# Kernel tuning notes

Hardware: AMD Instinct MI355X
Metric: run time of the kernel (lower is better)

The kernel has to match this reference:

```python
import jax, jax.numpy as jnp
import numpy as np

N, F, H, OUT, DDIM, E = 200000, 64, 256, 16, 768, 3200000


def setup_inputs() -> dict:
    key = jax.random.key(0)
    ks = jax.random.split(key, 20)
    s = lambda i, shp, sc=0.05: (jax.random.normal(ks[i], shp, jnp.float32) * sc)
    return dict(
        x=jax.random.normal(ks[0], (N, F), jnp.float32),
        edge_index=jax.random.randint(ks[1], (2, E), 0, N, dtype=jnp.int32),
        doc_feature=jax.random.normal(ks[2], (DDIM,), jnp.float32),
        pool_w=s(3, (F,)),
        init_weight=s(4, (F, F)),
        gru_w_ih=s(5, (3 * F, F)), gru_w_hh=s(6, (3 * F, F)),
        gru_b_ih=s(7, (3 * F,)), gru_b_hh=s(8, (3 * F,)),
        gnn_fc_w=s(9, (H, F)), gnn_fc_b=s(10, (H,)),
        doc_fc_w=s(11, (H, DDIM)), doc_fc_b=s(12, (H,)),
        ln_g=jnp.ones((2 * H,), jnp.float32), ln_b=jnp.zeros((2 * H,), jnp.float32),
        fusion_w=s(13, (H, 2 * H)), fusion_b=s(14, (H,)),
        task_w=s(15, (OUT, H)), task_b=s(16, (OUT,)),
        time_w=s(17, (1, H)), time_b=s(18, (1,)),
    )


def _forward(x, doc_feature, pool_w, init_weight, gru_w_ih, gru_w_hh, gru_b_ih,
             gru_b_hh, gnn_fc_w, gnn_fc_b, doc_fc_w, doc_fc_b, ln_g, ln_b,
             fusion_w, fusion_b, task_w, task_b, time_w, time_b, edge_index):
    n, f = x.shape
    # --- EvolveGCNH: TopK pooling, k = f since ratio = in_channels/num_nodes ---
    score = x @ pool_w / jnp.linalg.norm(pool_w)             # [n]
    top_s, perm = jax.lax.top_k(score, f)
    x_tilde = x[perm] * jnp.tanh(top_s)[:, None]             # [f, f]
    # --- single-step GRU; hidden state = previous GCN weight (detached) ---
    h0 = jax.lax.stop_gradient(init_weight)                  # [f, f]
    gx = x_tilde @ gru_w_ih.T + gru_b_ih                     # [f, 3f]
    gh = h0 @ gru_w_hh.T + gru_b_hh
    xr, xz, xn = jnp.split(gx, 3, axis=1)
    hr, hz, hn = jnp.split(gh, 3, axis=1)
    r = jax.nn.sigmoid(xr + hr)
    z = jax.nn.sigmoid(xz + hz)
    nc = jnp.tanh(xn + r * hn)
    W = (1.0 - z) * nc + z * h0                              # evolved weight [f, f]
    # --- GCNConv with fixed W: sym-norm adjacency with self loops ---
    xw = x @ W                                               # [n, f]
    loop = jnp.arange(n, dtype=edge_index.dtype)
    row = jnp.concatenate([edge_index[0], loop])
    col = jnp.concatenate([edge_index[1], loop])
    deg = jax.ops.segment_sum(jnp.ones_like(col, dtype=x.dtype), col, num_segments=n)
    dis = jnp.where(deg > 0, jax.lax.rsqrt(jnp.maximum(deg, 1e-12)), 0.0)
    norm = dis[row] * dis[col]                               # [E+n]
    x_gnn = jax.ops.segment_sum(xw[row] * norm[:, None], col, num_segments=n)  # [n, f]
    # --- global mean pool (batch is all zeros -> single graph) ---
    pooled = jnp.mean(x_gnn, axis=0, keepdims=True)          # [1, f]
    g = pooled @ gnn_fc_w.T + gnn_fc_b                        # [1, H]
    d = jax.nn.relu(doc_feature @ doc_fc_w.T + doc_fc_b)[None, :]  # [1, H]
    fused = jnp.concatenate([g, d], axis=1)                   # [1, 2H]
    mu = jnp.mean(fused, axis=-1, keepdims=True)
    var = jnp.var(fused, axis=-1, keepdims=True)
    ln = (fused - mu) * jax.lax.rsqrt(var + 1e-5) * ln_g + ln_b
    h1 = jax.nn.relu(ln @ fusion_w.T + fusion_b)              # dropout = identity (eval)
    return (h1 @ task_w.T + task_b, h1 @ time_w.T + time_b)


def reference(x, edge_index, doc_feature, pool_w, init_weight, gru_w_ih, gru_w_hh,
              gru_b_ih, gru_b_hh, gnn_fc_w, gnn_fc_b, doc_fc_w, doc_fc_b, ln_g,
              ln_b, fusion_w, fusion_b, task_w, task_b, time_w, time_b):
    return _forward(x, doc_feature, pool_w, init_weight, gru_w_ih, gru_w_hh,
                    gru_b_ih, gru_b_hh, gnn_fc_w, gnn_fc_b, doc_fc_w, doc_fc_b,
                    ln_g, ln_b, fusion_w, fusion_b, task_w, task_b, time_w,
                    time_b, edge_index)
```

## Files before the change

kernel.cpp:

```cpp
#include <hip/hip_runtime.h>
#include <hip/hip_bf16.h>

#define NN    200000
#define EE    3200000
#define DDIMC 768

#define NI4   800000
#define HTH   1024
#define PARTW (25 * 12 * 8192)

#define BSZC  32768
#define BSHC  15
#define NBC   7
#define CCC   72
#define BSZR  16384
#define BSHR  14
#define NBR   13
#define CCR   40

#define NDBLK 782
#define XBLOCKS 1024
#define CAPL  4096

#define HB    64
#define HW    32768

#define P_PART  0
#define P_DEGM  P_PART
#define P_PARTM (P_DEGM + 114688)
#define PZERO_LEN 327680
#define P_HIST  PARTW
#define P_CANDN (P_HIST + 65536)
#define P_S8    (P_CANDN + 8)
#define ZERO_LEN (8 + 512)
#define P_FLAG  (P_S8 + 512)
#define P_THR   (P_FLAG + 8)
#define P_SV    (P_THR + 8)
#define P_D     (P_SV + 64)
#define P_DIS   (P_D + 256)
#define P_C     (P_DIS + NN)
#define P_SCORE (P_C + NN)
#define P_CKEY  (P_SCORE + NN)
#define P_CIDX  (P_CKEY + 4096)
#define P_XT    (P_CIDX + 4096)
#define P_WW    (P_XT + 4096)
#define P_G     (P_WW + 4096)
#define P_LNV   (P_G + 256)
#define P_H1    (P_LNV + 512)

__device__ __forceinline__ float ldf(const void* p, int i, int bf) {
  if (bf) return __bfloat162float(((const __hip_bfloat16*)p)[i]);
  return ((const float*)p)[i];
}
__device__ __forceinline__ void stf(void* p, int i, float v, int bf) {
  if (bf) ((__hip_bfloat16*)p)[i] = __float2bfloat16(v);
  else ((float*)p)[i] = v;
}
__device__ __forceinline__ float bfu(unsigned u) {
  return __uint_as_float(u << 16);
}
__device__ __forceinline__ float wsum(float v) {
#pragma unroll
  for (int m = 32; m >= 1; m >>= 1) v += __shfl_xor(v, m, 64);
  return v;
}
__device__ __forceinline__ int wsumi(int v) {
#pragma unroll
  for (int m = 32; m >= 1; m >>= 1) v += __shfl_xor(v, m, 64);
  return v;
}
__device__ __forceinline__ unsigned sortkey(float f) {
  unsigned u = __float_as_uint(f);
  return (u & 0x80000000u) ? ~u : (u | 0x80000000u);
}

__global__ void k_detect(const unsigned short* x16, int* flag) {
  __shared__ int cnt;
  if (threadIdx.x == 0) cnt = 0;
  __syncthreads();
  int ok = 0;
  for (int k = threadIdx.x; k < 512; k += 256) {
    unsigned short u = x16[2 * k];
    int e = (u >> 7) & 0xFF;
    if (u == 0 || (e >= 100 && e <= 150)) ok++;
  }
  atomicAdd(&cnt, ok);
  __syncthreads();
  if (threadIdx.x == 0) flag[0] = (cnt >= 400) ? 1 : 0;
}

__global__ void __launch_bounds__(HTH) k_hcol(const int* __restrict__ col,
                                              unsigned* __restrict__ degm) {
  __shared__ unsigned lh[BSZC / 2];
  int t = threadIdx.x;
  int b = blockIdx.x / CCC, j = blockIdx.x % CCC;
  for (int k = t; k < BSZC / 2; k += HTH) lh[k] = 0u;
  __syncthreads();
  int base = b << BSHC;
  const int4* c4 = (const int4*)col;
  const int stride = CCC * HTH;
  for (int i = j * HTH + t; i < NI4; i += 2 * stride) {
    int4 v0 = c4[i];
    int i2 = i + stride;
    int4 v1; v1.x = v1.y = v1.z = v1.w = -1;
    if (i2 < NI4) v1 = c4[i2];
    {
      int a0 = v0.x - base, a1 = v0.y - base, a2 = v0.z - base, a3 = v0.w - base;
      if ((unsigned)a0 < (unsigned)BSZC) atomicAdd(&lh[a0 >> 1], 1u << ((a0 & 1) * 16));
      if ((unsigned)a1 < (unsigned)BSZC) atomicAdd(&lh[a1 >> 1], 1u << ((a1 & 1) * 16));
      if ((unsigned)a2 < (unsigned)BSZC) atomicAdd(&lh[a2 >> 1], 1u << ((a2 & 1) * 16));
      if ((unsigned)a3 < (unsigned)BSZC) atomicAdd(&lh[a3 >> 1], 1u << ((a3 & 1) * 16));
    }
    {
      int a0 = v1.x - base, a1 = v1.y - base, a2 = v1.z - base, a3 = v1.w - base;
      if ((unsigned)a0 < (unsigned)BSZC) atomicAdd(&lh[a0 >> 1], 1u << ((a0 & 1) * 16));
      if ((unsigned)a1 < (unsigned)BSZC) atomicAdd(&lh[a1 >> 1], 1u << ((a1 & 1) * 16));
      if ((unsigned)a2 < (unsigned)BSZC) atomicAdd(&lh[a2 >> 1], 1u << ((a2 & 1) * 16));
      if ((unsigned)a3 < (unsigned)BSZC) atomicAdd(&lh[a3 >> 1], 1u << ((a3 & 1) * 16));
    }
  }
  __syncthreads();
  unsigned* dst = degm + (size_t)b * (BSZC / 2);
  for (int k = t; k < BSZC / 2; k += HTH) {
    unsigned v = lh[k];
    if (v) atomicAdd(&dst[k], v);
  }
}

__global__ void k_redA(const unsigned* __restrict__ degm, float* __restrict__ dis,
                       const void* docf, const void* dw, const void* db,
                       float* __restrict__ d, const int* flagp) {
  if (blockIdx.x < NDBLK) {
    int i = blockIdx.x * 256 + threadIdx.x;
    if (i < NN) {
      unsigned w_ = degm[i >> 1];
      int deg = 1 + (int)((w_ >> ((i & 1) * 16)) & 0xffffu);
      dis[i] = rsqrtf((float)deg);
    }
  } else {
    int flag = flagp[0];
    int o = (blockIdx.x - NDBLK) * 4 + (threadIdx.x >> 6);
    int lane = threadIdx.x & 63;
    float acc = 0.f;
    for (int k = lane; k < DDIMC; k += 64) acc += ldf(docf, k, flag) * ldf(dw, o * DDIMC + k, flag);
    acc = wsum(acc);
    if (lane == 0) d[o] = fmaxf(acc + ldf(db, o, flag), 0.0f);
  }
}

__global__ void __launch_bounds__(HTH) k_hrow(const int* __restrict__ row, const int* __restrict__ col,
                                              const float* __restrict__ dis,
                                              float* __restrict__ partm) {
  __shared__ float lh[BSZR];
  int t = threadIdx.x;
  int b = blockIdx.x / CCR, j = blockIdx.x % CCR;
  for (int k = t; k < BSZR; k += HTH) lh[k] = 0.f;
  __syncthreads();
  int base = b << BSHR;
  const int4* r4 = (const int4*)row;
  const int4* c4 = (const int4*)col;
  const int stride = CCR * HTH;
  for (int i = j * HTH + t; i < NI4; i += 2 * stride) {
    int4 r0 = r4[i];
    int4 c0 = c4[i];
    int i2 = i + stride;
    int4 r1; r1.x = r1.y = r1.z = r1.w = -1;
    int4 c1; c1.x = c1.y = c1.z = c1.w = 0;
    if (i2 < NI4) { r1 = r4[i2]; c1 = c4[i2]; }
    {
      int a0 = r0.x - base, a1 = r0.y - base, a2 = r0.z - base, a3 = r0.w - base;
      if ((unsigned)a0 < (unsigned)BSZR) atomicAdd(&lh[a0], dis[c0.x]);
      if ((unsigned)a1 < (unsigned)BSZR) atomicAdd(&lh[a1], dis[c0.y]);
      if ((unsigned)a2 < (unsigned)BSZR) atomicAdd(&lh[a2], dis[c0.z]);
      if ((unsigned)a3 < (unsigned)BSZR) atomicAdd(&lh[a3], dis[c0.w]);
    }
    {
      int a0 = r1.x - base, a1 = r1.y - base, a2 = r1.z - base, a3 = r1.w - base;
      if ((unsigned)a0 < (unsigned)BSZR) atomicAdd(&lh[a0], dis[c1.x]);
      if ((unsigned)a1 < (unsigned)BSZR) atomicAdd(&lh[a1], dis[c1.y]);
      if ((unsigned)a2 < (unsigned)BSZR) atomicAdd(&lh[a2], dis[c1.z]);
      if ((unsigned)a3 < (unsigned)BSZR) atomicAdd(&lh[a3], dis[c1.w]);
    }
  }
  __syncthreads();
  float* dst = partm + (size_t)b * BSZR;
  for (int k = t; k < BSZR; k += HTH) {
    float v = lh[k];
    if (v != 0.f) atomicAdd(&dst[k], v);
  }
}

__global__ void k_redB(const float* __restrict__ partm, const float* __restrict__ dis,
                       float* __restrict__ c) {
  int i = blockIdx.x * 256 + threadIdx.x;
  if (i < NN) {
    float dv = dis[i];
    c[i] = dv * partm[i] + dv * dv;
  }
}

__global__ void k_x(const void* x, const void* pw, const float* __restrict__ c,
                    float* __restrict__ score,
                    float* __restrict__ s8, const int* flagp) {
  __shared__ float sred[4][64];
  int flag = flagp[0];
  int t = threadIdx.x;
  int lane = t & 63;
  int w = t >> 6;
  int wid = (blockIdx.x * 256 + t) >> 6;
  int nw = (gridDim.x * 256) >> 6;

  if (flag) {
    int g  = lane >> 3;
    int c0 = (lane & 7) * 8;
    float pwv[8];
#pragma unroll
    for (int j = 0; j < 8; j++) pwv[j] = ldf(pw, c0 + j, 1);
    float s = 0.f;
#pragma unroll
    for (int j = 0; j < 8; j++) s += pwv[j] * pwv[j];
    float inv = 1.0f / sqrtf(wsum(s) * 0.125f);
    float sacc[8] = {0.f, 0.f, 0.f, 0.f, 0.f, 0.f, 0.f, 0.f};
    const uint4* x4 = (const uint4*)x;
    for (int r0 = wid * 8; r0 < NN; r0 += nw * 8) {
      int r = r0 + g;
      uint4 u = x4[r * 8 + (lane & 7)];
      float xv[8] = { bfu(u.x & 0xffff), bfu(u.x >> 16),
                      bfu(u.y & 0xffff), bfu(u.y >> 16),
                      bfu(u.z & 0xffff), bfu(u.z >> 16),
                      bfu(u.w & 0xffff), bfu(u.w >> 16) };
      float dot = 0.f;
#pragma unroll
      for (int j = 0; j < 8; j++) dot += xv[j] * pwv[j];
      dot += __shfl_xor(dot, 1, 64);
      dot += __shfl_xor(dot, 2, 64);
      dot += __shfl_xor(dot, 4, 64);
      float cr = c[r];
#pragma unroll
      for (int j = 0; j < 8; j++) sacc[j] += cr * xv[j];
      if ((lane & 7) == 0) score[r] = dot * inv;
    }
#pragma unroll
    for (int j = 0; j < 8; j++) {
      sacc[j] += __shfl_xor(sacc[j], 8, 64);
      sacc[j] += __shfl_xor(sacc[j], 16, 64);
      sacc[j] += __shfl_xor(sacc[j], 32, 64);
    }
    if (lane < 8) {
#pragma unroll
      for (int j = 0; j < 8; j++) sred[w][lane * 8 + j] = sacc[j];
    }
  } else {
    int g  = lane >> 4;
    int c0 = (lane & 15) * 4;
    float pwv[4];
#pragma unroll
    for (int j = 0; j < 4; j++) pwv[j] = ((const float*)pw)[c0 + j];
    float s = 0.f;
#pragma unroll
    for (int j = 0; j < 4; j++) s += pwv[j] * pwv[j];
    float inv = 1.0f / sqrtf(wsum(s) * (1.f / 16.f));
    float sacc[4] = {0.f, 0.f, 0.f, 0.f};
    const float4* x4 = (const float4*)x;
    for (int r0 = wid * 4; r0 < NN; r0 += nw * 4) {
      int r = r0 + g;
      float4 v = x4[r * 16 + (lane & 15)];
      float xv[4] = { v.x, v.y, v.z, v.w };
      float dot = 0.f;
#pragma unroll
      for (int j = 0; j < 4; j++) dot += xv[j] * pwv[j];
      dot += __shfl_xor(dot, 1, 64);
      dot += __shfl_xor(dot, 2, 64);
      dot += __shfl_xor(dot, 4, 64);
      dot += __shfl_xor(dot, 8, 64);
      float cr = c[r];
#pragma unroll
      for (int j = 0; j < 4; j++) sacc[j] += cr * xv[j];
      if ((lane & 15) == 0) score[r] = dot * inv;
    }
#pragma unroll
    for (int j = 0; j < 4; j++) {
      sacc[j] += __shfl_xor(sacc[j], 16, 64);
      sacc[j] += __shfl_xor(sacc[j], 32, 64);
    }
    if (lane < 16) {
#pragma unroll
      for (int j = 0; j < 4; j++) sred[w][lane * 4 + j] = sacc[j];
    }
  }
  __syncthreads();
  if (w == 0)
    atomicAdd(&s8[(blockIdx.x & 7) * 64 + lane],
              sred[0][lane] + sred[1][lane] + sred[2][lane] + sred[3][lane]);
}

__global__ void __launch_bounds__(1024) k_hist(const float* __restrict__ score,
                                               unsigned* __restrict__ part) {
  __shared__ unsigned lh[HW];
  int t = threadIdx.x;
  for (int k = t; k < HW; k += 1024) lh[k] = 0u;
  __syncthreads();
  int r0 = blockIdx.x * (NN / HB);
  int r1 = r0 + (NN / HB);
  for (int i = r0 + t; i < r1; i += 1024) {
    unsigned b = sortkey(score[i]) >> 16;
    atomicAdd(&lh[b >> 1], 1u << ((b & 1) * 16));
  }
  __syncthreads();
  unsigned* dst = part + (size_t)blockIdx.x * HW;
  for (int k = t; k < HW; k += 1024) dst[k] = lh[k];
}

__global__ void k_redH(const unsigned* __restrict__ part, int* __restrict__ hist) {
  int w = blockIdx.x * 256 + threadIdx.x;
  unsigned lo = 0, hi = 0;
  for (int b = 0; b < HB; b++) {
    unsigned v = part[(size_t)b * HW + w];
    lo += v & 0xffffu;
    hi += v >> 16;
  }
  hist[2 * w]     = (int)lo;
  hist[2 * w + 1] = (int)hi;
}

__global__ void k_thresh(const int* __restrict__ hist, int* __restrict__ thrB,
                         const float* __restrict__ s8, float* __restrict__ svec) {
  __shared__ int part[256];
  __shared__ int segl[256];
  __shared__ int res2[2];
  int t = threadIdx.x, w = t >> 6, lane = t & 63;
  if (t < 64) {
    float a = 0.f;
    for (int r = 0; r < 8; r++) a += s8[r * 64 + t];
    svec[t] = a;
  }
  for (int m = w; m < 256; m += 4) {
    const int* hb = &hist[m * 256];
    int a = hb[lane] + hb[lane + 64] + hb[lane + 128] + hb[lane + 192];
    a = wsumi(a);
    if (lane == 0) part[m] = a;
  }
  __syncthreads();
  if (t == 0) {
    int acc = 0, seg = 0, above = 0;
    for (int b = 255; b >= 0; b--) {
      if (acc + part[b] >= 64) { seg = b; above = acc; break; }
      acc += part[b];
    }
    res2[0] = seg; res2[1] = above;
  }
  __syncthreads();
  segl[t] = hist[res2[0] * 256 + t];
  __syncthreads();
  if (t == 0) {
    int acc = res2[1], B = res2[0] * 256;
    for (int j = 255; j >= 0; j--) {
      acc += segl[j];
      if (acc >= 64) { B = res2[0] * 256 + j; break; }
    }
    thrB[0] = B;
  }
}

__global__ void k_collect(const float* __restrict__ score, const int* __restrict__ thrB,
                          int* __restrict__ candn, unsigned* __restrict__ ckey,
                          int* __restrict__ cidx) {
  int i = blockIdx.x * blockDim.x + threadIdx.x;
  if (i >= NN) return;
  unsigned u = sortkey(score[i]);
  if ((int)(u >> 16) >= thrB[0]) {
    int p = atomicAdd(candn, 1);
    if (p < CAPL) { ckey[p] = u; cidx[p] = i; }
  }
}

__global__ void k_top(const int* __restrict__ candn, const unsigned* __restrict__ ckey,
                      const int* __restrict__ cidx, const void* x,
                      float* __restrict__ xt, const int* flagp) {
  __shared__ unsigned long long keys[CAPL];
  __shared__ int perm[64];
  __shared__ float ts[64];
  int flag = flagp[0];
  int t = threadIdx.x;
  int M = candn[0];
  if (M > CAPL) M = CAPL;
  for (int j = t; j < M; j += 256)
    keys[j] = (((unsigned long long)ckey[j]) << 32) |
              (unsigned long long)(0xFFFFFFFFu - (unsigned)cidx[j]);
  __syncthreads();
  for (int j = t; j < M; j += 256) {
    unsigned long long k = keys[j];
    int rank = 0;
    for (int i = 0; i < M; i++) rank += (keys[i] > k) ? 1 : 0;
    if (rank < 64) {
      unsigned ku = (unsigned)(k >> 32);
      unsigned idx = 0xFFFFFFFFu - (unsigned)(k & 0xFFFFFFFFu);
      perm[rank] = (int)idx;
      unsigned bits = (ku & 0x80000000u) ? (ku ^ 0x80000000u) : ~ku;
      ts[rank] = tanhf(__uint_as_float(bits));
    }
  }
  __syncthreads();
  for (int q = t; q < 4096; q += 256) {
    int j = q >> 6, f = q & 63;
    xt[q] = ldf(x, perm[j] * 64 + f, flag) * ts[j];
  }
}

#define GS 193
__device__ __forceinline__ void stage_w(const void* src, float* dst, int flag, int t) {
  if (flag) {
    const uint4* s4 = (const uint4*)src;
    for (int k = t; k < 1536; k += 256) {
      uint4 u = s4[k];
      int e = k << 3; int o = e >> 6, f = e & 63;
      float* d = &dst[f * GS + o];
      d[0]      = bfu(u.x & 0xffff); d[GS]     = bfu(u.x >> 16);
      d[2 * GS] = bfu(u.y & 0xffff); d[3 * GS] = bfu(u.y >> 16);
      d[4 * GS] = bfu(u.z & 0xffff); d[5 * GS] = bfu(u.z >> 16);
      d[6 * GS] = bfu(u.w & 0xffff); d[7 * GS] = bfu(u.w >> 16);
    }
  } else {
    const float4* s4 = (const float4*)src;
    for (int k = t; k < 3072; k += 256) {
      float4 v = s4[k];
      int e = k << 2; int o = e >> 6, f = e & 63;
      float* d = &dst[f * GS + o];
      d[0] = v.x; d[GS] = v.y; d[2 * GS] = v.z; d[3 * GS] = v.w;
    }
  }
}

__global__ void k_gru(const float* __restrict__ xt, const void* h0g, const void* wihg,
                      const void* whhg, const void* bihg, const void* bhhg,
                      float* __restrict__ Wout, const int* flagp) {
  __shared__ float wb1[64 * GS];
  __shared__ float wb2[64 * GS];
  __shared__ float xtr[256];
  __shared__ float h0r[256];
  int flag = flagp[0];
  int t = threadIdx.x;
  int j0 = blockIdx.x * 4;
  { int jj = t >> 6, f = t & 63;
    xtr[t] = xt[(j0 + jj) * 64 + f];
    h0r[t] = ldf(h0g, (j0 + jj) * 64 + f, flag); }
  stage_w(wihg, wb1, flag, t);
  stage_w(whhg, wb2, flag, t);
  __syncthreads();
  int jl = t >> 6, c2 = t & 63;
  float xr = 0, xz = 0, xn = 0, hr = 0, hz = 0, hn = 0;
#pragma unroll 4
  for (int f = 0; f < 64; f++) {
    float xv = xtr[jl * 64 + f];
    float hv = h0r[jl * 64 + f];
    const float* w1 = &wb1[f * GS];
    const float* w2 = &wb2[f * GS];
    xr += xv * w1[c2]; xz += xv * w1[64 + c2]; xn += xv * w1[128 + c2];
    hr += hv * w2[c2]; hz += hv * w2[64 + c2]; hn += hv * w2[128 + c2];
  }
  xr += ldf(bihg, c2, flag); xz += ldf(bihg, 64 + c2, flag); xn += ldf(bihg, 128 + c2, flag);
  hr += ldf(bhhg, c2, flag); hz += ldf(bhhg, 64 + c2, flag); hn += ldf(bhhg, 128 + c2, flag);
  float rg = 1.f / (1.f + expf(-(xr + hr)));
  float zg = 1.f / (1.f + expf(-(xz + hz)));
  float nc = tanhf(xn + rg * hn);
  Wout[(j0 + jl) * 64 + c2] = (1.f - zg) * nc + zg * h0r[jl * 64 + c2];
}

__global__ void k_g(const float* __restrict__ svec, const float* __restrict__ Wm,
                    const void* gw, const void* gb, float* __restrict__ g,
                    const int* flagp) {
  __shared__ float pooled[64];
  int flag = flagp[0];
  int t = threadIdx.x, w = t >> 6, lane = t & 63;
  if (t < 64) {
    float a = 0.f;
    for (int f = 0; f < 64; f++) a += svec[f] * Wm[f * 64 + t];
    pooled[t] = a * (1.0f / (float)NN);
  }
  __syncthreads();
  int o = blockIdx.x * 4 + w;
  float acc = pooled[lane] * ldf(gw, o * 64 + lane, flag);
  acc = wsum(acc);
  if (lane == 0) g[o] = acc + ldf(gb, o, flag);
}

__global__ void k_ln(const float* __restrict__ g, const float* __restrict__ d,
                     const void* lng, const void* lnb, float* __restrict__ lnv,
                     const int* flagp) {
  __shared__ float red[256];
  __shared__ float stats[2];
  int flag = flagp[0];
  int t = threadIdx.x;
  float v0 = g[t], v1 = d[t];
  red[t] = v0 + v1; __syncthreads();
  for (int s = 128; s > 0; s >>= 1) { if (t < s) red[t] += red[t + s]; __syncthreads(); }
  if (t == 0) stats[0] = red[0];
  __syncthreads();
  red[t] = v0 * v0 + v1 * v1; __syncthreads();
  for (int s = 128; s > 0; s >>= 1) { if (t < s) red[t] += red[t + s]; __syncthreads(); }
  if (t == 0) stats[1] = red[0];
  __syncthreads();
  float mu = stats[0] * (1.f / 512.f);
  float var = stats[1] * (1.f / 512.f) - mu * mu;
  float istd = rsqrtf(var + 1e-5f);
  lnv[t]       = (v0 - mu) * istd * ldf(lng, t, flag)       + ldf(lnb, t, flag);
  lnv[t + 256] = (v1 - mu) * istd * ldf(lng, t + 256, flag) + ldf(lnb, t + 256, flag);
}

__global__ void k_fuse(const float* __restrict__ lnv, const void* fw, const void* fb,
                       float* __restrict__ h1, const int* flagp) {
  __shared__ float lv[512];
  int flag = flagp[0];
  int t = threadIdx.x, w = t >> 6, lane = t & 63;
  lv[t] = lnv[t]; lv[t + 256] = lnv[t + 256];
  __syncthreads();
  int o = blockIdx.x * 4 + w;
  float acc = 0.f;
  if (flag) {
    uint4 u = *((const uint4*)((const unsigned short*)fw + o * 512) + lane);
    const float* l = &lv[lane * 8];
    acc = bfu(u.x & 0xffff) * l[0] + bfu(u.x >> 16) * l[1]
        + bfu(u.y & 0xffff) * l[2] + bfu(u.y >> 16) * l[3]
        + bfu(u.z & 0xffff) * l[4] + bfu(u.z >> 16) * l[5]
        + bfu(u.w & 0xffff) * l[6] + bfu(u.w >> 16) * l[7];
  } else {
    const float4* fv = (const float4*)((const float*)fw + o * 512);
    float4 a = fv[lane * 2], b = fv[lane * 2 + 1];
    const float* l = &lv[lane * 8];
    acc = a.x * l[0] + a.y * l[1] + a.z * l[2] + a.w * l[3]
        + b.x * l[4] + b.y * l[5] + b.z * l[6] + b.w * l[7];
  }
  acc = wsum(acc);
  if (lane == 0) h1[o] = fmaxf(acc + ldf(fb, o, flag), 0.0f);
}

__global__ void k_out(const float* __restrict__ h1, const void* tw, const void* tb,
                      const void* tmw, const void* tmb, void* out, const int* flagp) {
  int flag = flagp[0];
  int t = threadIdx.x, w = t >> 6, lane = t & 63;
  int o = blockIdx.x * 4 + w;
  if (o >= 17) return;
  float acc = 0.f;
  if (o < 16) { for (int k = lane; k < 256; k += 64) acc += h1[k] * ldf(tw, o * 256 + k, flag); }
  else        { for (int k = lane; k < 256; k += 64) acc += h1[k] * ldf(tmw, k, flag); }
  acc = wsum(acc);
  if (lane == 0) {
    float bias = (o < 16) ? ldf(tb, o, flag) : ldf(tmb, 0, flag);
    stf(out, o, acc + bias, flag);
  }
}

extern "C" void kernel_launch(void* const* d_in, const int* in_sizes, int n_in,
                              void* d_out, int out_size, void* d_ws, size_t ws_size,
                              hipStream_t stream) {
  const void* x    = d_in[0];
  const int*  ei   = (const int*)d_in[1];
  const void* docf = d_in[2];
  const void* pw   = d_in[3];
  const void* h0   = d_in[4];
  const void* wih  = d_in[5];
  const void* whh  = d_in[6];
  const void* bih  = d_in[7];
  const void* bhh  = d_in[8];
  const void* gw   = d_in[9];
  const void* gb   = d_in[10];
  const void* dw   = d_in[11];
  const void* db   = d_in[12];
  const void* lng  = d_in[13];
  const void* lnb  = d_in[14];
  const void* fw   = d_in[15];
  const void* fb   = d_in[16];
  const void* tw   = d_in[17];
  const void* tb   = d_in[18];
  const void* tmw  = d_in[19];
  const void* tmb  = d_in[20];

  const int* row = ei;
  const int* col = ei + EE;

  float* wsf = (float*)d_ws;
  int*   wsi = (int*)d_ws;

  hipMemsetAsync(wsi + P_PART, 0, (size_t)PZERO_LEN * 4, stream);
  hipMemsetAsync(wsi + P_CANDN, 0, (size_t)ZERO_LEN * 4, stream);
  k_detect<<<1, 256, 0, stream>>>((const unsigned short*)x, wsi + P_FLAG);
  k_hcol<<<NBC * CCC, HTH, 0, stream>>>(col, (unsigned*)(wsi + P_DEGM));
  k_redA<<<NDBLK + 64, 256, 0, stream>>>((const unsigned*)(wsi + P_DEGM), wsf + P_DIS,
                                         docf, dw, db, wsf + P_D, wsi + P_FLAG);
  k_hrow<<<NBR * CCR, HTH, 0, stream>>>(row, col, wsf + P_DIS, wsf + P_PARTM);
  k_redB<<<NDBLK, 256, 0, stream>>>(wsf + P_PARTM, wsf + P_DIS, wsf + P_C);
  k_x<<<XBLOCKS, 256, 0, stream>>>(x, pw, wsf + P_C, wsf + P_SCORE,
                                   wsf + P_S8, wsi + P_FLAG);
  k_hist<<<HB, 1024, 0, stream>>>(wsf + P_SCORE, (unsigned*)(wsi + P_PART));
  k_redH<<<HW / 256, 256, 0, stream>>>((const unsigned*)(wsi + P_PART), wsi + P_HIST);
  k_thresh<<<1, 256, 0, stream>>>(wsi + P_HIST, wsi + P_THR, wsf + P_S8, wsf + P_SV);
  k_collect<<<NDBLK, 256, 0, stream>>>(wsf + P_SCORE, wsi + P_THR, wsi + P_CANDN,
                                       (unsigned*)(wsi + P_CKEY), wsi + P_CIDX);
  k_top<<<1, 256, 0, stream>>>(wsi + P_CANDN, (const unsigned*)(wsi + P_CKEY),
                               wsi + P_CIDX, x, wsf + P_XT, wsi + P_FLAG);
  k_gru<<<16, 256, 0, stream>>>(wsf + P_XT, h0, wih, whh, bih, bhh, wsf + P_WW, wsi + P_FLAG);
  k_g<<<64, 256, 0, stream>>>(wsf + P_SV, wsf + P_WW, gw, gb, wsf + P_G, wsi + P_FLAG);
  k_ln<<<1, 256, 0, stream>>>(wsf + P_G, wsf + P_D, lng, lnb, wsf + P_LNV, wsi + P_FLAG);
  k_fuse<<<64, 256, 0, stream>>>(wsf + P_LNV, fw, fb, wsf + P_H1, wsi + P_FLAG);
  k_out<<<5, 256, 0, stream>>>(wsf + P_H1, tw, tb, tmw, tmb, d_out, wsi + P_FLAG);
}
```

Before: 323.0 us.

## Spread histogram flush atomics across eight replicas and widen top-k block

```diff
diff --git a/kernel.cpp b/kernel.cpp
--- a/kernel.cpp
+++ b/kernel.cpp
@@ -13,10 +13,12 @@
 #define BSHC  15
 #define NBC   7
 #define CCC   72
+#define DEGC  (NBC * (BSZC / 2))
 #define BSZR  16384
 #define BSHR  14
 #define NBR   13
 #define CCR   40
+#define PARTC (NBR * BSZR)
 
 #define NDBLK 782
 #define XBLOCKS 1024
@@ -26,9 +28,10 @@
 #define HW    32768
 
 #define P_PART  0
-#define P_DEGM  P_PART
-#define P_PARTM (P_DEGM + 114688)
-#define PZERO_LEN 327680
+#define P_DEGM  0
+#define P_PARTM 0
+#define ZLEN1   (8 * DEGC)
+#define ZLEN2   (8 * PARTC)
 #define P_HIST  PARTW
 #define P_CANDN (P_HIST + 65536)
 #define P_S8    (P_CANDN + 8)
@@ -120,7 +123,7 @@
     }
   }
   __syncthreads();
-  unsigned* dst = degm + (size_t)b * (BSZC / 2);
+  unsigned* dst = degm + (size_t)(j & 7) * DEGC + (size_t)b * (BSZC / 2);
   for (int k = t; k < BSZC / 2; k += HTH) {
     unsigned v = lh[k];
     if (v) atomicAdd(&dst[k], v);
@@ -133,8 +136,13 @@
   if (blockIdx.x < NDBLK) {
     int i = blockIdx.x * 256 + threadIdx.x;
     if (i < NN) {
-      unsigned w_ = degm[i >> 1];
-      int deg = 1 + (int)((w_ >> ((i & 1) * 16)) & 0xffffu);
+      int sh = (i & 1) * 16;
+      int deg = 1;
+#pragma unroll
+      for (int p = 0; p < 8; p++) {
+        unsigned w_ = degm[(size_t)p * DEGC + (i >> 1)];
+        deg += (int)((w_ >> sh) & 0xffffu);
+      }
       dis[i] = rsqrtf((float)deg);
     }
   } else {
@@ -183,7 +191,7 @@
     }
   }
   __syncthreads();
-  float* dst = partm + (size_t)b * BSZR;
+  float* dst = partm + (size_t)(j & 7) * PARTC + (size_t)b * BSZR;
   for (int k = t; k < BSZR; k += HTH) {
     float v = lh[k];
     if (v != 0.f) atomicAdd(&dst[k], v);
@@ -194,8 +202,11 @@
                        float* __restrict__ c) {
   int i = blockIdx.x * 256 + threadIdx.x;
   if (i < NN) {
+    float s = 0.f;
+#pragma unroll
+    for (int p = 0; p < 8; p++) s += partm[(size_t)p * PARTC + i];
     float dv = dis[i];
-    c[i] = dv * partm[i] + dv * dv;
+    c[i] = dv * s + dv * dv;
   }
 }
 
@@ -374,7 +385,8 @@
   }
 }
 
-__global__ void k_top(const int* __restrict__ candn, const unsigned* __restrict__ ckey,
+__global__ void __launch_bounds__(1024) k_top(const int* __restrict__ candn,
+                      const unsigned* __restrict__ ckey,
                       const int* __restrict__ cidx, const void* x,
                       float* __restrict__ xt, const int* flagp) {
   __shared__ unsigned long long keys[CAPL];
@@ -384,11 +396,11 @@
   int t = threadIdx.x;
   int M = candn[0];
   if (M > CAPL) M = CAPL;
-  for (int j = t; j < M; j += 256)
+  for (int j = t; j < M; j += 1024)
     keys[j] = (((unsigned long long)ckey[j]) << 32) |
               (unsigned long long)(0xFFFFFFFFu - (unsigned)cidx[j]);
   __syncthreads();
-  for (int j = t; j < M; j += 256) {
+  for (int j = t; j < M; j += 1024) {
     unsigned long long k = keys[j];
     int rank = 0;
     for (int i = 0; i < M; i++) rank += (keys[i] > k) ? 1 : 0;
@@ -401,7 +413,7 @@
     }
   }
   __syncthreads();
-  for (int q = t; q < 4096; q += 256) {
+  for (int q = t; q < 4096; q += 1024) {
     int j = q >> 6, f = q & 63;
     xt[q] = ldf(x, perm[j] * 64 + f, flag) * ts[j];
   }
@@ -581,12 +593,13 @@
   float* wsf = (float*)d_ws;
   int*   wsi = (int*)d_ws;
 
-  hipMemsetAsync(wsi + P_PART, 0, (size_t)PZERO_LEN * 4, stream);
+  hipMemsetAsync(wsi + P_DEGM, 0, (size_t)ZLEN1 * 4, stream);
   hipMemsetAsync(wsi + P_CANDN, 0, (size_t)ZERO_LEN * 4, stream);
   k_detect<<<1, 256, 0, stream>>>((const unsigned short*)x, wsi + P_FLAG);
   k_hcol<<<NBC * CCC, HTH, 0, stream>>>(col, (unsigned*)(wsi + P_DEGM));
   k_redA<<<NDBLK + 64, 256, 0, stream>>>((const unsigned*)(wsi + P_DEGM), wsf + P_DIS,
                                          docf, dw, db, wsf + P_D, wsi + P_FLAG);
+  hipMemsetAsync(wsi + P_PARTM, 0, (size_t)ZLEN2 * 4, stream);
   k_hrow<<<NBR * CCR, HTH, 0, stream>>>(row, col, wsf + P_DIS, wsf + P_PARTM);
   k_redB<<<NDBLK, 256, 0, stream>>>(wsf + P_PARTM, wsf + P_DIS, wsf + P_C);
   k_x<<<XBLOCKS, 256, 0, stream>>>(x, pw, wsf + P_C, wsf + P_SCORE,
@@ -596,8 +609,8 @@
   k_thresh<<<1, 256, 0, stream>>>(wsi + P_HIST, wsi + P_THR, wsf + P_S8, wsf + P_SV);
   k_collect<<<NDBLK, 256, 0, stream>>>(wsf + P_SCORE, wsi + P_THR, wsi + P_CANDN,
                                        (unsigned*)(wsi + P_CKEY), wsi + P_CIDX);
-  k_top<<<1, 256, 0, stream>>>(wsi + P_CANDN, (const unsigned*)(wsi + P_CKEY),
-                               wsi + P_CIDX, x, wsf + P_XT, wsi + P_FLAG);
+  k_top<<<1, 1024, 0, stream>>>(wsi + P_CANDN, (const unsigned*)(wsi + P_CKEY),
+                                wsi + P_CIDX, x, wsf + P_XT, wsi + P_FLAG);
   k_gru<<<16, 256, 0, stream>>>(wsf + P_XT, h0, wih, whh, bih, bhh, wsf + P_WW, wsi + P_FLAG);
   k_g<<<64, 256, 0, stream>>>(wsf + P_SV, wsf + P_WW, gw, gb, wsf + P_G, wsi + P_FLAG);
   k_ln<<<1, 256, 0, stream>>>(wsf + P_G, wsf + P_D, lng, lnb, wsf + P_LNV, wsi + P_FLAG);
```

New measurement: 325.3 us. About the same (+0.7%).
